# Optimization experiments

Measured on AMD Instinct MI355X. Metric: run time of the kernel, lower is better.

## Reference

```python
import jax, jax.numpy as jnp
import numpy as np

B, S, IN, H = 16, 512, 512, 256
TAU_TRACE = 20.0
TAU_MEM = 20.0
DECAY_TRACE = float(np.exp(-1.0 / TAU_TRACE))  # exp_convolve decay
DECAY_MEM = float(np.exp(-1.0 / TAU_MEM))      # leaky-integrator dynamics decay
LR = 0.01                                       # plasticity learning rate
W_MAX = 1.0                                     # soft upper bound on fast weights


def setup_inputs() -> dict:
    key = jax.random.key(0)
    k1, k2 = jax.random.split(key)
    x = jax.random.normal(k1, (B, S, IN), dtype=jnp.float32)
    # xavier_uniform with gain=sqrt(2) on W of shape [2H, IN]
    lim = float(np.sqrt(2.0) * np.sqrt(6.0 / (2 * H + IN)))
    W = jax.random.uniform(k2, (2 * H, IN), dtype=jnp.float32, minval=-lim, maxval=lim)
    return {"x": x, "W": W}


def reference(x, W):
    # i = x @ W^T : [B, S, 2H], then split into key/value input currents
    i = jnp.einsum('bsi,hi->bsh', x, W)
    ik, iv = jnp.split(i, 2, axis=2)  # each [B, S, H]
    bsz = x.shape[0]
    h = W.shape[0] // 2

    def step(carry, inp):
        kv, vv, kt, vt, mem = carry
        ik_t, iv_t = inp  # [B, H] each
        # key dynamics (leaky integrator + tanh)
        kv = DECAY_MEM * kv + ik_t
        key = jnp.tanh(kv)
        # memory readout: 0.2 * (key.unsqueeze(1) * mem).sum(2) == 0.2 * mem @ key
        ikv = 0.2 * jnp.einsum('bij,bj->bi', mem, key)
        # value dynamics
        vv = DECAY_MEM * vv + iv_t + ikv
        val = jnp.tanh(vv)
        # exponential traces
        kt = DECAY_TRACE * kt + (1.0 - DECAY_TRACE) * key
        vt = DECAY_TRACE * vt + (1.0 - DECAY_TRACE) * val
        # soft-bounded Hebbian outer-product fast-weight update
        mem = mem + LR * (vt[:, :, None] * kt[:, None, :]) * (W_MAX - mem)
        return (kv, vv, kt, vt, mem), (key, val)

    z = jnp.zeros((bsz, h), x.dtype)
    mem0 = jnp.zeros((bsz, h, h), x.dtype)
    (_, _, _, _, mem), (keys, vals) = jax.lax.scan(
        step, (z, z, z, z, mem0),
        (jnp.swapaxes(ik, 0, 1), jnp.swapaxes(iv, 0, 1)))  # scan over time
    return mem, jnp.swapaxes(keys, 0, 1), jnp.swapaxes(vals, 0, 1)
```

## Files before the change

kernel.cpp:

```cpp
#include <hip/hip_runtime.h>

#define BB 16
#define SS 512
#define KIN 512
#define H 256

typedef float v2f __attribute__((ext_vector_type(2)));

constexpr float DECAY = 0.951229424500714f;
constexpr float OMD   = 0.048770575499286f;
constexpr float LR    = 0.01f;
constexpr float WMAX  = 1.0f;

__device__ __forceinline__ float fast_tanh(float x) {
    float e = __expf(2.f * x);
    return 1.f - __fdividef(2.f, e + 1.f);
}

__device__ __forceinline__ float allsum32(float x) {
    int t;
    t = __builtin_amdgcn_update_dpp(0, __float_as_int(x), 0x121, 0xf, 0xf, false);
    x += __int_as_float(t);
    t = __builtin_amdgcn_update_dpp(0, __float_as_int(x), 0x122, 0xf, 0xf, false);
    x += __int_as_float(t);
    t = __builtin_amdgcn_update_dpp(0, __float_as_int(x), 0x124, 0xf, 0xf, false);
    x += __int_as_float(t);
    t = __builtin_amdgcn_update_dpp(0, __float_as_int(x), 0x128, 0xf, 0xf, false);
    x += __int_as_float(t);
    t = __builtin_amdgcn_ds_swizzle(__float_as_int(x), 0x401F);
    x += __int_as_float(t);
    return x;
}

__global__ __launch_bounds__(256) void gemm_xwT(const float* __restrict__ X,
                                                const float* __restrict__ W,
                                                float* __restrict__ ik_out,
                                                float* __restrict__ iv_t) {
    __shared__ float As[16][68];
    __shared__ float Bs[16][68];
    const int m0 = blockIdx.y * 64;
    const int n0 = blockIdx.x * 64;
    const int tid = threadIdx.x;
    const int r  = tid >> 2;
    const int cg = tid & 3;
    const int tx = tid & 15;
    const int ty = tid >> 4;
    float acc[4][4] = {};
    for (int k0 = 0; k0 < KIN; k0 += 16) {
        float4 av = *(const float4*)&X[(size_t)(m0 + r) * KIN + k0 + cg * 4];
        float4 bv = *(const float4*)&W[(size_t)(n0 + r) * KIN + k0 + cg * 4];
        __syncthreads();
        As[cg*4+0][r] = av.x; As[cg*4+1][r] = av.y; As[cg*4+2][r] = av.z; As[cg*4+3][r] = av.w;
        Bs[cg*4+0][r] = bv.x; Bs[cg*4+1][r] = bv.y; Bs[cg*4+2][r] = bv.z; Bs[cg*4+3][r] = bv.w;
        __syncthreads();
#pragma unroll
        for (int kk = 0; kk < 16; ++kk) {
            float4 a = *(const float4*)&As[kk][ty * 4];
            float4 b = *(const float4*)&Bs[kk][tx * 4];
            float ar[4] = {a.x, a.y, a.z, a.w};
            float br[4] = {b.x, b.y, b.z, b.w};
#pragma unroll
            for (int i = 0; i < 4; ++i)
#pragma unroll
                for (int j = 0; j < 4; ++j) acc[i][j] += ar[i] * br[j];
        }
    }
    if (n0 < 256) {
#pragma unroll
        for (int i = 0; i < 4; ++i) {
            float4 o = make_float4(acc[i][0], acc[i][1], acc[i][2], acc[i][3]);
            *(float4*)&ik_out[(size_t)(m0 + ty * 4 + i) * 256 + n0 + tx * 4] = o;
        }
    } else {
        const int b  = m0 >> 9;
        const int s0 = (m0 & 511) + ty * 4;
#pragma unroll
        for (int j = 0; j < 4; ++j) {
            float4 o = make_float4(acc[0][j], acc[1][j], acc[2][j], acc[3][j]);
            *(float4*)&iv_t[((size_t)b * H + (n0 - 256 + tx * 4 + j)) * SS + s0] = o;
        }
    }
}

__global__ __launch_bounds__(64) void key_scan(const float* __restrict__ ik,
                                               float* __restrict__ keys) {
    const int idx = blockIdx.x * 64 + threadIdx.x;
    const int b   = idx >> 8;
    const int col = idx & 255;
    const float* c  = ik + (size_t)b * SS * 256 + col;
    float* ko = keys + (size_t)b * SS * H + col;
    float kv = 0.f;
    constexpr int D = 32;
    float ib[D];
#pragma unroll
    for (int j = 0; j < D; ++j) ib[j] = c[(size_t)j * 256];
    for (int t = 0; t < SS; t += D) {
#pragma unroll
        for (int j = 0; j < D; ++j) {
            float v = ib[j];
            int tn = t + D + j; if (tn > SS - 1) tn = SS - 1;
            ib[j] = c[(size_t)tn * 256];
            kv = DECAY * kv + v;
            ko[(size_t)(t + j) * H] = fast_tanh(kv);
        }
    }
}

__global__ __launch_bounds__(256) void value_scan(const float* __restrict__ keys,
                                                  const float* __restrict__ iv_t,
                                                  float* __restrict__ mem_out,
                                                  float* __restrict__ vals) {
    const int tid  = threadIdx.x;
    const int wave = tid >> 6;
    const int lane = tid & 63;
    const int half = lane >> 5;
    const int sub  = lane & 31;
    const int b    = blockIdx.x & 15;
    const int rg   = blockIdx.x >> 4;
    const int row  = rg * 8 + wave * 2 + half;
    const int so   = sub * 8;

    const float* kb  = keys + (size_t)b * SS * H;
    const float* ivb = iv_t + ((size_t)b * H + row) * SS;
    float* valout = vals + (size_t)b * SS * H;

    const v2f DEC2 = {DECAY, DECAY};
    const v2f OMD2 = {OMD, OMD};
    const v2f W2   = {WMAX, WMAX};

    v2f mem2[4] = {{0.f,0.f},{0.f,0.f},{0.f,0.f},{0.f,0.f}};
    v2f ktr2[4] = {{0.f,0.f},{0.f,0.f},{0.f,0.f},{0.f,0.f}};
    float vv = 0.f, vt = 0.f;

    float4 kA[8], kB[8];
#pragma unroll
    for (int j = 0; j < 8; ++j) {
        kA[j] = *(const float4*)&kb[(size_t)j * H + so];
        kB[j] = *(const float4*)&kb[(size_t)j * H + so + 4];
    }
    float4 ivA0 = *(const float4*)&ivb[0];
    float4 ivA1 = *(const float4*)&ivb[4];
    float4 ivB0 = *(const float4*)&ivb[8];
    float4 ivB1 = *(const float4*)&ivb[12];

    auto step = [&](int t, int j, float civ) {
        float4 kc0 = kA[j], kc1 = kB[j];
        int tn = t + 8 + j; if (tn > SS - 1) tn = SS - 1;
        kA[j] = *(const float4*)&kb[(size_t)tn * H + so];
        kB[j] = *(const float4*)&kb[(size_t)tn * H + so + 4];
        v2f kc2[4] = {{kc0.x, kc0.y}, {kc0.z, kc0.w}, {kc1.x, kc1.y}, {kc1.z, kc1.w}};
        v2f p2 = mem2[0] * kc2[0] + mem2[1] * kc2[1]
               + mem2[2] * kc2[2] + mem2[3] * kc2[3];
        float ikv = 0.2f * allsum32(p2.x + p2.y);
        vv = DECAY * vv + civ + ikv;
        float valv = fast_tanh(vv);
        vt = DECAY * vt + OMD * valv;
        if (sub == 0) valout[(size_t)(t + j) * H + row] = valv;
        v2f c2 = {LR * vt, LR * vt};
#pragma unroll
        for (int q = 0; q < 4; ++q) {
            ktr2[q] = DEC2 * ktr2[q] + OMD2 * kc2[q];
            mem2[q] += (c2 * ktr2[q]) * (W2 - mem2[q]);
        }
    };

    for (int t0 = 0; t0 < SS; t0 += 16) {
        {
            float iva[8] = {ivA0.x, ivA0.y, ivA0.z, ivA0.w, ivA1.x, ivA1.y, ivA1.z, ivA1.w};
            int tp = t0 + 16; if (tp > SS - 8) tp = SS - 8;
            ivA0 = *(const float4*)&ivb[tp];
            ivA1 = *(const float4*)&ivb[tp + 4];
#pragma unroll
            for (int j = 0; j < 8; ++j) step(t0, j, iva[j]);
        }
        {
            float ivc[8] = {ivB0.x, ivB0.y, ivB0.z, ivB0.w, ivB1.x, ivB1.y, ivB1.z, ivB1.w};
            int tp = t0 + 24; if (tp > SS - 8) tp = SS - 8;
            ivB0 = *(const float4*)&ivb[tp];
            ivB1 = *(const float4*)&ivb[tp + 4];
#pragma unroll
            for (int j = 0; j < 8; ++j) step(t0 + 8, j, ivc[j]);
        }
    }

    float* mo = &mem_out[((size_t)b * H + row) * H + so];
    *(float4*)&mo[0] = make_float4(mem2[0].x, mem2[0].y, mem2[1].x, mem2[1].y);
    *(float4*)&mo[4] = make_float4(mem2[2].x, mem2[2].y, mem2[3].x, mem2[3].y);
}

extern "C" void kernel_launch(void* const* d_in, const int* in_sizes, int n_in,
                              void* d_out, int out_size, void* d_ws, size_t ws_size,
                              hipStream_t stream) {
    const float* x = (const float*)d_in[0];
    const float* W = (const float*)d_in[1];
    float* out = (float*)d_out;
    float* mem_out = out;
    float* keys = out + (size_t)BB * H * H;
    float* vals = keys + (size_t)BB * SS * H;
    float* ik   = (float*)d_ws;
    float* iv_t = ik + (size_t)BB * SS * 256;

    dim3 gb(8, 128);
    gemm_xwT<<<gb, 256, 0, stream>>>(x, W, ik, iv_t);
    key_scan<<<64, 64, 0, stream>>>(ik, keys);
    value_scan<<<512, 256, 0, stream>>>(keys, iv_t, mem_out, vals);
}
```

Measured before the change: 259.5 us.

## Reparameterize fast-weight memory as u=1-mem and fold key sums into value input

```diff
diff --git a/kernel.cpp b/kernel.cpp
--- a/kernel.cpp
+++ b/kernel.cpp
@@ -10,26 +10,33 @@
 constexpr float DECAY = 0.951229424500714f;
 constexpr float OMD   = 0.048770575499286f;
 constexpr float LR    = 0.01f;
-constexpr float WMAX  = 1.0f;
 
 __device__ __forceinline__ float fast_tanh(float x) {
     float e = __expf(2.f * x);
     return 1.f - __fdividef(2.f, e + 1.f);
 }
 
-__device__ __forceinline__ float allsum32(float x) {
+__device__ __forceinline__ v2f pk_mul(v2f a, v2f b) {
+    v2f d; asm("v_pk_mul_f32 %0, %1, %2" : "=v"(d) : "v"(a), "v"(b)); return d;
+}
+__device__ __forceinline__ v2f pk_fma(v2f a, v2f b, v2f c) {
+    v2f d; asm("v_pk_fma_f32 %0, %1, %2, %3" : "=v"(d) : "v"(a), "v"(b), "v"(c)); return d;
+}
+
+__device__ __forceinline__ void half_sum32(float x, float& s_lo, float& s_hi) {
     int t;
-    t = __builtin_amdgcn_update_dpp(0, __float_as_int(x), 0x121, 0xf, 0xf, false);
-    x += __int_as_float(t);
-    t = __builtin_amdgcn_update_dpp(0, __float_as_int(x), 0x122, 0xf, 0xf, false);
-    x += __int_as_float(t);
-    t = __builtin_amdgcn_update_dpp(0, __float_as_int(x), 0x124, 0xf, 0xf, false);
-    x += __int_as_float(t);
-    t = __builtin_amdgcn_update_dpp(0, __float_as_int(x), 0x128, 0xf, 0xf, false);
-    x += __int_as_float(t);
-    t = __builtin_amdgcn_ds_swizzle(__float_as_int(x), 0x401F);
-    x += __int_as_float(t);
-    return x;
+    t = __builtin_amdgcn_update_dpp(0, __float_as_int(x), 0x111, 0xf, 0xf, false);
+    x += __int_as_float(t);
+    t = __builtin_amdgcn_update_dpp(0, __float_as_int(x), 0x112, 0xf, 0xf, false);
+    x += __int_as_float(t);
+    t = __builtin_amdgcn_update_dpp(0, __float_as_int(x), 0x114, 0xf, 0xf, false);
+    x += __int_as_float(t);
+    t = __builtin_amdgcn_update_dpp(0, __float_as_int(x), 0x118, 0xf, 0xf, false);
+    x += __int_as_float(t);
+    t = __builtin_amdgcn_update_dpp(0, __float_as_int(x), 0x142, 0xa, 0xf, false);
+    x += __int_as_float(t);
+    s_lo = __int_as_float(__builtin_amdgcn_readlane(__float_as_int(x), 31));
+    s_hi = __int_as_float(__builtin_amdgcn_readlane(__float_as_int(x), 63));
 }
 
 __global__ __launch_bounds__(256) void gemm_xwT(const float* __restrict__ X,
@@ -106,6 +113,31 @@
     }
 }
 
+__global__ __launch_bounds__(256) void ksum_kernel(const float* __restrict__ keys,
+                                                   float* __restrict__ ksum) {
+    const int gwave = (blockIdx.x * 256 + threadIdx.x) >> 6;
+    const int lane  = threadIdx.x & 63;
+    const int b = gwave >> 9;
+    const int t = gwave & 511;
+    float4 k = *(const float4*)&keys[((size_t)b * SS + t) * H + lane * 4];
+    float s = k.x + k.y + k.z + k.w;
+#pragma unroll
+    for (int off = 1; off < 64; off <<= 1) s += __shfl_xor(s, off);
+    if (lane == 0) ksum[(size_t)b * SS + t] = 0.2f * s;
+}
+
+__global__ __launch_bounds__(128) void fold_kernel(const float* __restrict__ ksum,
+                                                   float* __restrict__ iv_t) {
+    const int b   = blockIdx.x >> 8;
+    const int row = blockIdx.x & 255;
+    const int t   = threadIdx.x * 4;
+    float4 ks = *(const float4*)&ksum[(size_t)b * SS + t];
+    float* p = &iv_t[((size_t)b * H + row) * SS + t];
+    float4 iv = *(const float4*)p;
+    iv.x += ks.x; iv.y += ks.y; iv.z += ks.z; iv.w += ks.w;
+    *(float4*)p = iv;
+}
+
 __global__ __launch_bounds__(256) void value_scan(const float* __restrict__ keys,
                                                   const float* __restrict__ iv_t,
                                                   float* __restrict__ mem_out,
@@ -120,72 +152,82 @@
     const int row  = rg * 8 + wave * 2 + half;
     const int so   = sub * 8;
 
-    const float* kb  = keys + (size_t)b * SS * H;
-    const float* ivb = iv_t + ((size_t)b * H + row) * SS;
-    float* valout = vals + (size_t)b * SS * H;
+    const float* kp  = keys + (size_t)b * SS * H + so;
+    const float* ivp = iv_t + ((size_t)b * H + row) * SS;
+    float* vp = vals + (size_t)b * SS * H + row;
 
     const v2f DEC2 = {DECAY, DECAY};
     const v2f OMD2 = {OMD, OMD};
-    const v2f W2   = {WMAX, WMAX};
-
-    v2f mem2[4] = {{0.f,0.f},{0.f,0.f},{0.f,0.f},{0.f,0.f}};
-    v2f ktr2[4] = {{0.f,0.f},{0.f,0.f},{0.f,0.f},{0.f,0.f}};
+
+    v2f u[4]   = {{1.f,1.f},{1.f,1.f},{1.f,1.f},{1.f,1.f}};
+    v2f ktr[4] = {{0.f,0.f},{0.f,0.f},{0.f,0.f},{0.f,0.f}};
     float vv = 0.f, vt = 0.f;
 
-    float4 kA[8], kB[8];
-#pragma unroll
-    for (int j = 0; j < 8; ++j) {
-        kA[j] = *(const float4*)&kb[(size_t)j * H + so];
-        kB[j] = *(const float4*)&kb[(size_t)j * H + so + 4];
-    }
-    float4 ivA0 = *(const float4*)&ivb[0];
-    float4 ivA1 = *(const float4*)&ivb[4];
-    float4 ivB0 = *(const float4*)&ivb[8];
-    float4 ivB1 = *(const float4*)&ivb[12];
-
-    auto step = [&](int t, int j, float civ) {
-        float4 kc0 = kA[j], kc1 = kB[j];
-        int tn = t + 8 + j; if (tn > SS - 1) tn = SS - 1;
-        kA[j] = *(const float4*)&kb[(size_t)tn * H + so];
-        kB[j] = *(const float4*)&kb[(size_t)tn * H + so + 4];
-        v2f kc2[4] = {{kc0.x, kc0.y}, {kc0.z, kc0.w}, {kc1.x, kc1.y}, {kc1.z, kc1.w}};
-        v2f p2 = mem2[0] * kc2[0] + mem2[1] * kc2[1]
-               + mem2[2] * kc2[2] + mem2[3] * kc2[3];
-        float ikv = 0.2f * allsum32(p2.x + p2.y);
-        vv = DECAY * vv + civ + ikv;
-        float valv = fast_tanh(vv);
-        vt = DECAY * vt + OMD * valv;
-        if (sub == 0) valout[(size_t)(t + j) * H + row] = valv;
-        v2f c2 = {LR * vt, LR * vt};
-#pragma unroll
-        for (int q = 0; q < 4; ++q) {
-            ktr2[q] = DEC2 * ktr2[q] + OMD2 * kc2[q];
-            mem2[q] += (c2 * ktr2[q]) * (W2 - mem2[q]);
-        }
-    };
-
-    for (int t0 = 0; t0 < SS; t0 += 16) {
-        {
-            float iva[8] = {ivA0.x, ivA0.y, ivA0.z, ivA0.w, ivA1.x, ivA1.y, ivA1.z, ivA1.w};
-            int tp = t0 + 16; if (tp > SS - 8) tp = SS - 8;
-            ivA0 = *(const float4*)&ivb[tp];
-            ivA1 = *(const float4*)&ivb[tp + 4];
-#pragma unroll
-            for (int j = 0; j < 8; ++j) step(t0, j, iva[j]);
-        }
-        {
-            float ivc[8] = {ivB0.x, ivB0.y, ivB0.z, ivB0.w, ivB1.x, ivB1.y, ivB1.z, ivB1.w};
-            int tp = t0 + 24; if (tp > SS - 8) tp = SS - 8;
-            ivB0 = *(const float4*)&ivb[tp];
-            ivB1 = *(const float4*)&ivb[tp + 4];
-#pragma unroll
-            for (int j = 0; j < 8; ++j) step(t0 + 8, j, ivc[j]);
-        }
-    }
+    v2f kR[8][4];
+#pragma unroll
+    for (int j = 0; j < 8; ++j)
+#pragma unroll
+        for (int q = 0; q < 4; ++q)
+            kR[j][q] = *(const v2f*)(kp + (size_t)j * H + q * 2);
+    kp += 8 * H;
+
+    float4 ivc0 = *(const float4*)(ivp);
+    float4 ivc1 = *(const float4*)(ivp + 4);
+    ivp += 8;
+
+#define VS_STEP(J, RELOAD, KOFF)                                               \
+    {                                                                          \
+        v2f kc0 = kR[J][0], kc1 = kR[J][1], kc2 = kR[J][2], kc3 = kR[J][3];    \
+        if (RELOAD) {                                                          \
+            kR[J][0] = *(const v2f*)(kp + (KOFF) * H + 0);                     \
+            kR[J][1] = *(const v2f*)(kp + (KOFF) * H + 2);                     \
+            kR[J][2] = *(const v2f*)(kp + (KOFF) * H + 4);                     \
+            kR[J][3] = *(const v2f*)(kp + (KOFF) * H + 6);                     \
+        }                                                                      \
+        v2f p2 = pk_mul(u[0], kc0);                                            \
+        p2 = pk_fma(u[1], kc1, p2);                                            \
+        p2 = pk_fma(u[2], kc2, p2);                                            \
+        p2 = pk_fma(u[3], kc3, p2);                                            \
+        float slo, shi;                                                        \
+        half_sum32(p2.x + p2.y, slo, shi);                                     \
+        float ps = half ? shi : slo;                                           \
+        float civ = (J) < 4 ? ((J)==0?ivc0.x:(J)==1?ivc0.y:(J)==2?ivc0.z:ivc0.w)\
+                            : ((J)==4?ivc1.x:(J)==5?ivc1.y:(J)==6?ivc1.z:ivc1.w);\
+        vv = DECAY * vv + civ;                                                 \
+        vv = __builtin_fmaf(-0.2f, ps, vv);                                    \
+        float valv = fast_tanh(vv);                                            \
+        vt = DECAY * vt + OMD * valv;                                          \
+        if (sub == 0) vp[(size_t)((J) & 3) * H] = valv;                        \
+        float an = -LR * vt;                                                   \
+        v2f an2 = {an, an};                                                    \
+        ktr[0] = pk_fma(DEC2, ktr[0], pk_mul(OMD2, kc0));                      \
+        ktr[1] = pk_fma(DEC2, ktr[1], pk_mul(OMD2, kc1));                      \
+        ktr[2] = pk_fma(DEC2, ktr[2], pk_mul(OMD2, kc2));                      \
+        ktr[3] = pk_fma(DEC2, ktr[3], pk_mul(OMD2, kc3));                      \
+        u[0] = pk_fma(pk_mul(an2, ktr[0]), u[0], u[0]);                        \
+        u[1] = pk_fma(pk_mul(an2, ktr[1]), u[1], u[1]);                        \
+        u[2] = pk_fma(pk_mul(an2, ktr[2]), u[2], u[2]);                        \
+        u[3] = pk_fma(pk_mul(an2, ktr[3]), u[3], u[3]);                        \
+    }
+
+    for (int t0 = 0; t0 < SS - 8; t0 += 8) {
+        float4 ivn0 = *(const float4*)(ivp);
+        float4 ivn1 = *(const float4*)(ivp + 4);
+        ivp += 8;
+        VS_STEP(0, true, 0) VS_STEP(1, true, 1) VS_STEP(2, true, 2) VS_STEP(3, true, 3)
+        kp += 4 * H; vp += 4 * H;
+        VS_STEP(4, true, 0) VS_STEP(5, true, 1) VS_STEP(6, true, 2) VS_STEP(7, true, 3)
+        kp += 4 * H; vp += 4 * H;
+        ivc0 = ivn0; ivc1 = ivn1;
+    }
+    VS_STEP(0, false, 0) VS_STEP(1, false, 0) VS_STEP(2, false, 0) VS_STEP(3, false, 0)
+    vp += 4 * H;
+    VS_STEP(4, false, 0) VS_STEP(5, false, 0) VS_STEP(6, false, 0) VS_STEP(7, false, 0)
+#undef VS_STEP
 
     float* mo = &mem_out[((size_t)b * H + row) * H + so];
-    *(float4*)&mo[0] = make_float4(mem2[0].x, mem2[0].y, mem2[1].x, mem2[1].y);
-    *(float4*)&mo[4] = make_float4(mem2[2].x, mem2[2].y, mem2[3].x, mem2[3].y);
+    *(float4*)&mo[0] = make_float4(1.f - u[0].x, 1.f - u[0].y, 1.f - u[1].x, 1.f - u[1].y);
+    *(float4*)&mo[4] = make_float4(1.f - u[2].x, 1.f - u[2].y, 1.f - u[3].x, 1.f - u[3].y);
 }
 
 extern "C" void kernel_launch(void* const* d_in, const int* in_sizes, int n_in,
@@ -199,9 +241,12 @@
     float* vals = keys + (size_t)BB * SS * H;
     float* ik   = (float*)d_ws;
     float* iv_t = ik + (size_t)BB * SS * 256;
+    float* ksum = ik;
 
     dim3 gb(8, 128);
     gemm_xwT<<<gb, 256, 0, stream>>>(x, W, ik, iv_t);
     key_scan<<<64, 64, 0, stream>>>(ik, keys);
+    ksum_kernel<<<2048, 256, 0, stream>>>(keys, ksum);
+    fold_kernel<<<4096, 128, 0, stream>>>(ksum, iv_t);
     value_scan<<<512, 256, 0, stream>>>(keys, iv_t, mem_out, vals);
 }
```

New measurement: 267.8 us. 1.03x slower.

## Map one mem row per wave with 4 columns per lane in value scan

Applied to the files above, without the earlier changes.

```diff
diff --git a/kernel.cpp b/kernel.cpp
--- a/kernel.cpp
+++ b/kernel.cpp
@@ -5,31 +5,30 @@
 #define KIN 512
 #define H 256
 
-typedef float v2f __attribute__((ext_vector_type(2)));
-
 constexpr float DECAY = 0.951229424500714f;
 constexpr float OMD   = 0.048770575499286f;
 constexpr float LR    = 0.01f;
-constexpr float WMAX  = 1.0f;
 
 __device__ __forceinline__ float fast_tanh(float x) {
     float e = __expf(2.f * x);
     return 1.f - __fdividef(2.f, e + 1.f);
 }
 
-__device__ __forceinline__ float allsum32(float x) {
+__device__ __forceinline__ float wave_sum64(float x) {
     int t;
-    t = __builtin_amdgcn_update_dpp(0, __float_as_int(x), 0x121, 0xf, 0xf, false);
-    x += __int_as_float(t);
-    t = __builtin_amdgcn_update_dpp(0, __float_as_int(x), 0x122, 0xf, 0xf, false);
-    x += __int_as_float(t);
-    t = __builtin_amdgcn_update_dpp(0, __float_as_int(x), 0x124, 0xf, 0xf, false);
-    x += __int_as_float(t);
-    t = __builtin_amdgcn_update_dpp(0, __float_as_int(x), 0x128, 0xf, 0xf, false);
-    x += __int_as_float(t);
-    t = __builtin_amdgcn_ds_swizzle(__float_as_int(x), 0x401F);
-    x += __int_as_float(t);
-    return x;
+    t = __builtin_amdgcn_update_dpp(0, __float_as_int(x), 0x111, 0xf, 0xf, false);
+    x += __int_as_float(t);
+    t = __builtin_amdgcn_update_dpp(0, __float_as_int(x), 0x112, 0xf, 0xf, false);
+    x += __int_as_float(t);
+    t = __builtin_amdgcn_update_dpp(0, __float_as_int(x), 0x114, 0xf, 0xf, false);
+    x += __int_as_float(t);
+    t = __builtin_amdgcn_update_dpp(0, __float_as_int(x), 0x118, 0xf, 0xf, false);
+    x += __int_as_float(t);
+    t = __builtin_amdgcn_update_dpp(0, __float_as_int(x), 0x142, 0xa, 0xf, false);
+    x += __int_as_float(t);
+    t = __builtin_amdgcn_update_dpp(0, __float_as_int(x), 0x143, 0xc, 0xf, false);
+    x += __int_as_float(t);
+    return __int_as_float(__builtin_amdgcn_readlane(__float_as_int(x), 63));
 }
 
 __global__ __launch_bounds__(256) void gemm_xwT(const float* __restrict__ X,
@@ -106,86 +105,98 @@
     }
 }
 
-__global__ __launch_bounds__(256) void value_scan(const float* __restrict__ keys,
-                                                  const float* __restrict__ iv_t,
-                                                  float* __restrict__ mem_out,
-                                                  float* __restrict__ vals) {
+__global__ __launch_bounds__(256, 4) void value_scan(const float* __restrict__ keys,
+                                                     const float* __restrict__ iv_t,
+                                                     float* __restrict__ mem_out,
+                                                     float* __restrict__ vals) {
     const int tid  = threadIdx.x;
     const int wave = tid >> 6;
     const int lane = tid & 63;
-    const int half = lane >> 5;
-    const int sub  = lane & 31;
     const int b    = blockIdx.x & 15;
     const int rg   = blockIdx.x >> 4;
-    const int row  = rg * 8 + wave * 2 + half;
-    const int so   = sub * 8;
-
-    const float* kb  = keys + (size_t)b * SS * H;
-    const float* ivb = iv_t + ((size_t)b * H + row) * SS;
-    float* valout = vals + (size_t)b * SS * H;
-
-    const v2f DEC2 = {DECAY, DECAY};
-    const v2f OMD2 = {OMD, OMD};
-    const v2f W2   = {WMAX, WMAX};
-
-    v2f mem2[4] = {{0.f,0.f},{0.f,0.f},{0.f,0.f},{0.f,0.f}};
-    v2f ktr2[4] = {{0.f,0.f},{0.f,0.f},{0.f,0.f},{0.f,0.f}};
-    float vv = 0.f, vt = 0.f;
+    const int row  = rg * 4 + wave;
+
+    const float* kp  = keys + (size_t)b * SS * H + lane * 4;
+    const float* ivp = iv_t + ((size_t)b * H + row) * SS;
+    float* vp = vals + (size_t)b * SS * H + row;
+
+    float mem[4] = {0.f, 0.f, 0.f, 0.f};
+    float ktr[4] = {0.f, 0.f, 0.f, 0.f};
+    float vv = 0.f, vt = 0.f, stash = 0.f;
 
     float4 kA[8], kB[8];
 #pragma unroll
-    for (int j = 0; j < 8; ++j) {
-        kA[j] = *(const float4*)&kb[(size_t)j * H + so];
-        kB[j] = *(const float4*)&kb[(size_t)j * H + so + 4];
-    }
-    float4 ivA0 = *(const float4*)&ivb[0];
-    float4 ivA1 = *(const float4*)&ivb[4];
-    float4 ivB0 = *(const float4*)&ivb[8];
-    float4 ivB1 = *(const float4*)&ivb[12];
-
-    auto step = [&](int t, int j, float civ) {
-        float4 kc0 = kA[j], kc1 = kB[j];
-        int tn = t + 8 + j; if (tn > SS - 1) tn = SS - 1;
-        kA[j] = *(const float4*)&kb[(size_t)tn * H + so];
-        kB[j] = *(const float4*)&kb[(size_t)tn * H + so + 4];
-        v2f kc2[4] = {{kc0.x, kc0.y}, {kc0.z, kc0.w}, {kc1.x, kc1.y}, {kc1.z, kc1.w}};
-        v2f p2 = mem2[0] * kc2[0] + mem2[1] * kc2[1]
-               + mem2[2] * kc2[2] + mem2[3] * kc2[3];
-        float ikv = 0.2f * allsum32(p2.x + p2.y);
-        vv = DECAY * vv + civ + ikv;
-        float valv = fast_tanh(vv);
-        vt = DECAY * vt + OMD * valv;
-        if (sub == 0) valout[(size_t)(t + j) * H + row] = valv;
-        v2f c2 = {LR * vt, LR * vt};
-#pragma unroll
-        for (int q = 0; q < 4; ++q) {
-            ktr2[q] = DEC2 * ktr2[q] + OMD2 * kc2[q];
-            mem2[q] += (c2 * ktr2[q]) * (W2 - mem2[q]);
-        }
-    };
-
-    for (int t0 = 0; t0 < SS; t0 += 16) {
+    for (int j = 0; j < 8; ++j) kA[j] = *(const float4*)(kp + (size_t)j * H);
+#pragma unroll
+    for (int j = 0; j < 8; ++j) kB[j] = *(const float4*)(kp + (size_t)(8 + j) * H);
+    kp += 16 * H;
+    float4 iA0 = *(const float4*)(ivp + 0);
+    float4 iA1 = *(const float4*)(ivp + 4);
+    float4 iB0 = *(const float4*)(ivp + 8);
+    float4 iB1 = *(const float4*)(ivp + 12);
+    ivp += 16;
+
+    for (int t2 = 0; t2 < 32; ++t2) {
+        const float* kq  = (t2 < 31) ? kp  : (kp - 16 * H);
+        const float* ivq = (t2 < 31) ? ivp : (ivp - 16);
+        float4 nA0 = *(const float4*)(ivq + 0);
+        float4 nA1 = *(const float4*)(ivq + 4);
+        float4 nB0 = *(const float4*)(ivq + 8);
+        float4 nB1 = *(const float4*)(ivq + 12);
+
         {
-            float iva[8] = {ivA0.x, ivA0.y, ivA0.z, ivA0.w, ivA1.x, ivA1.y, ivA1.z, ivA1.w};
-            int tp = t0 + 16; if (tp > SS - 8) tp = SS - 8;
-            ivA0 = *(const float4*)&ivb[tp];
-            ivA1 = *(const float4*)&ivb[tp + 4];
-#pragma unroll
-            for (int j = 0; j < 8; ++j) step(t0, j, iva[j]);
+            float ivs[8] = {iA0.x, iA0.y, iA0.z, iA0.w, iA1.x, iA1.y, iA1.z, iA1.w};
+#pragma unroll
+            for (int j = 0; j < 8; ++j) {
+                float4 kc = kA[j];
+                kA[j] = *(const float4*)(kq + (size_t)j * H);
+                float p = mem[0] * kc.x + mem[1] * kc.y + mem[2] * kc.z + mem[3] * kc.w;
+                float s = wave_sum64(p);
+                vv = __builtin_fmaf(DECAY, vv, ivs[j]);
+                vv = __builtin_fmaf(0.2f, s, vv);
+                float valv = fast_tanh(vv);
+                vt = __builtin_fmaf(DECAY, vt, OMD * valv);
+                if (lane == j) stash = valv;
+                float c = LR * vt;
+                float kr[4] = {kc.x, kc.y, kc.z, kc.w};
+#pragma unroll
+                for (int q = 0; q < 4; ++q) {
+                    ktr[q] = __builtin_fmaf(DECAY, ktr[q], OMD * kr[q]);
+                    mem[q] = __builtin_fmaf(c * ktr[q], 1.f - mem[q], mem[q]);
+                }
+            }
         }
         {
-            float ivc[8] = {ivB0.x, ivB0.y, ivB0.z, ivB0.w, ivB1.x, ivB1.y, ivB1.z, ivB1.w};
-            int tp = t0 + 24; if (tp > SS - 8) tp = SS - 8;
-            ivB0 = *(const float4*)&ivb[tp];
-            ivB1 = *(const float4*)&ivb[tp + 4];
-#pragma unroll
-            for (int j = 0; j < 8; ++j) step(t0 + 8, j, ivc[j]);
-        }
-    }
-
-    float* mo = &mem_out[((size_t)b * H + row) * H + so];
-    *(float4*)&mo[0] = make_float4(mem2[0].x, mem2[0].y, mem2[1].x, mem2[1].y);
-    *(float4*)&mo[4] = make_float4(mem2[2].x, mem2[2].y, mem2[3].x, mem2[3].y);
+            float ivs[8] = {iB0.x, iB0.y, iB0.z, iB0.w, iB1.x, iB1.y, iB1.z, iB1.w};
+#pragma unroll
+            for (int j = 0; j < 8; ++j) {
+                float4 kc = kB[j];
+                kB[j] = *(const float4*)(kq + (size_t)(8 + j) * H);
+                float p = mem[0] * kc.x + mem[1] * kc.y + mem[2] * kc.z + mem[3] * kc.w;
+                float s = wave_sum64(p);
+                vv = __builtin_fmaf(DECAY, vv, ivs[j]);
+                vv = __builtin_fmaf(0.2f, s, vv);
+                float valv = fast_tanh(vv);
+                vt = __builtin_fmaf(DECAY, vt, OMD * valv);
+                if (lane == 8 + j) stash = valv;
+                float c = LR * vt;
+                float kr[4] = {kc.x, kc.y, kc.z, kc.w};
+#pragma unroll
+                for (int q = 0; q < 4; ++q) {
+                    ktr[q] = __builtin_fmaf(DECAY, ktr[q], OMD * kr[q]);
+                    mem[q] = __builtin_fmaf(c * ktr[q], 1.f - mem[q], mem[q]);
+                }
+            }
+        }
+        if (lane < 16) vp[(size_t)lane * H] = stash;
+        vp += 16 * H;
+        kp += 16 * H;
+        ivp += 16;
+        iA0 = nA0; iA1 = nA1; iB0 = nB0; iB1 = nB1;
+    }
+
+    *(float4*)&mem_out[((size_t)b * H + row) * H + lane * 4] =
+        make_float4(mem[0], mem[1], mem[2], mem[3]);
 }
 
 extern "C" void kernel_launch(void* const* d_in, const int* in_sizes, int n_in,
@@ -203,5 +214,5 @@
     dim3 gb(8, 128);
     gemm_xwT<<<gb, 256, 0, stream>>>(x, W, ik, iv_t);
     key_scan<<<64, 64, 0, stream>>>(ik, keys);
-    value_scan<<<512, 256, 0, stream>>>(keys, iv_t, mem_out, vals);
-}
+    value_scan<<<1024, 256, 0, stream>>>(keys, iv_t, mem_out, vals);
+}
```

Result: slower. 305.6 us (+17.8%).
